# Kernel optimization log

Measured on AMD Instinct MI355X. Metric: run time of the kernel, lower is better.

## Reference

```python
import jax, jax.numpy as jnp
import numpy as np

NUM_USERS, NUM_ITEMS, D = 100000, 200000, 128
B, LLEN, SLEN = 4096, 200, 50
NEG = -1e9


def setup_inputs() -> dict:
    key = jax.random.key(0)
    ks = jax.random.split(key, 10)
    w_range = float(np.sqrt(3.0 / D))
    return {
        "user_table": 0.01 * jax.random.normal(ks[0], (NUM_USERS, D), dtype=jnp.float32),
        "item_table": 0.01 * jax.random.normal(ks[1], (NUM_ITEMS, D), dtype=jnp.float32),
        "W1": jax.random.uniform(ks[2], (2 * D, 16), minval=-w_range, maxval=w_range, dtype=jnp.float32),
        "b1": jnp.zeros((16,), dtype=jnp.float32),
        "W2": jax.random.uniform(ks[3], (16, 1), minval=-w_range, maxval=w_range, dtype=jnp.float32),
        "b2": jnp.zeros((1,), dtype=jnp.float32),
        "user_inputs": jax.random.randint(ks[4], (B,), 0, NUM_USERS, dtype=jnp.int64) if jax.config.jax_enable_x64 else jax.random.randint(ks[4], (B,), 0, NUM_USERS, dtype=jnp.int32),
        "L_inputs": jax.random.randint(ks[5], (B, LLEN), 0, NUM_ITEMS, dtype=jnp.int32),
        "S_inputs": jax.random.randint(ks[6], (B, SLEN), 0, NUM_ITEMS, dtype=jnp.int32),
        "item_inputs": jax.random.randint(ks[7], (B,), 0, NUM_ITEMS, dtype=jnp.int32),
    }


def reference(user_table, item_table, W1, b1, W2, b2,
              user_inputs, L_inputs, S_inputs, item_inputs):
    def att_logits(x):  # x: [..., 2D] -> [...]
        h = jax.nn.relu(x @ W1 + b1)
        return (h @ W2 + b2)[..., 0]

    def masked_softmax(logits, mask):  # softmax over last axis restricted to mask
        logits = jnp.where(mask, logits, NEG)
        return jax.nn.softmax(logits, axis=-1)

    u_emb = user_table[user_inputs]                      # [B, D]

    # ---- long-term attention over L history ----
    L_mask = L_inputs >= 0                               # [B, L]
    L_idx = jnp.where(L_mask, L_inputs, 0)
    L_emb = item_table[L_idx]                            # [B, L, D]
    uL = jnp.concatenate([jnp.broadcast_to(u_emb[:, None, :], L_emb.shape), L_emb], axis=-1)  # [B, L, 2D]
    w1 = masked_softmax(att_logits(uL), L_mask)          # [B, L]
    u_long = jnp.einsum('bl,bld->bd', w1, L_emb)         # [B, D]

    # ---- short-term attention over [u_long] + S (L assumed nonempty) ----
    S_mask = S_inputs >= 0                               # [B, S]
    S_idx = jnp.where(S_mask, S_inputs, 0)
    S_emb = item_table[S_idx]                            # [B, S, D]
    seq = jnp.concatenate([u_long[:, None, :], S_emb], axis=1)   # [B, 1+S, D]
    seq_mask = jnp.concatenate([jnp.ones((seq.shape[0], 1), dtype=bool), S_mask], axis=1)
    uSeq = jnp.concatenate([jnp.broadcast_to(u_emb[:, None, :], seq.shape), seq], axis=-1)  # [B, 1+S, 2D]
    w2 = masked_softmax(att_logits(uSeq), seq_mask)      # [B, 1+S]
    user_hybrid = jnp.einsum('bs,bsd->bd', w2, seq)      # [B, D]

    # ---- score: bmm([B,1,D], [B,D,1]) -> [B,1,1] ----
    item_emb = item_table[item_inputs]                   # [B, D]
    score = jnp.sum(user_hybrid * item_emb, axis=-1)[:, None, None]
    return score
```

## Files before the change

kernel.cpp:

```cpp
#include <hip/hip_runtime.h>
#include <math.h>

#define D 128
#define LLEN 200
#define SLEN 50
#define CH 64
#define ESTR 132
#define NEG (-1e9f)

__device__ __forceinline__ float wave_red_sum(float v) {
#pragma unroll
  for (int m = 32; m >= 1; m >>= 1) v += __shfl_xor(v, m, 64);
  return v;
}
__device__ __forceinline__ float block_sum(float v, float* red) {
  v = wave_red_sum(v);
  if ((threadIdx.x & 63) == 0) red[threadIdx.x >> 6] = v;
  __syncthreads();
  v = red[0] + red[1] + red[2] + red[3];
  __syncthreads();
  return v;
}

#define GATHER_L(dst, IT, BASE)                          \
  do {                                                   \
    int s_ = tid + (IT);                                 \
    int gid_ = rows1[(BASE) + (s_ >> 5)];                \
    if (gid_ < 0) gid_ = 0;                              \
    dst = it4[(size_t)gid_ * 32 + (s_ & 31)];            \
  } while (0)

#define GATHER_S(dst, IT)                                \
  do {                                                   \
    int s_ = tid + (IT);                                 \
    int gid_ = rowsS[s_ >> 5];                           \
    if (gid_ < 0) gid_ = 0;                              \
    dst = it4[(size_t)gid_ * 32 + (s_ & 31)];            \
  } while (0)

#define STORE_L(src, IT)                                                    \
  do {                                                                      \
    int s_ = tid + (IT);                                                    \
    reinterpret_cast<float4*>(&ebuf[(s_ >> 5) * ESTR])[s_ & 31] = src;      \
  } while (0)

#define STORE_S(src, IT)                                                    \
  do {                                                                      \
    int s_ = tid + (IT);                                                    \
    reinterpret_cast<float4*>(&ebuf[((s_ >> 5) + 1) * ESTR])[s_ & 31] = src; \
  } while (0)

#define MATVEC_PHASE(CNT)                                                   \
  if (lane < (CNT)) {                                                       \
    float a0 = 0.f, a1 = 0.f, a2 = 0.f, a3 = 0.f;                           \
    const float4* er4 = reinterpret_cast<const float4*>(&ebuf[lane * ESTR]);\
    const float* wc = &W1[(size_t)D * 16 + 4 * w];                          \
    _Pragma("unroll 8")                                                     \
    for (int k = 0; k < 32; ++k) {                                          \
      float4 e = er4[k];                                                    \
      const float* wr = wc + k * 64;            \
      a0 = fmaf(e.x, wr[0],  a0); a1 = fmaf(e.x, wr[1],  a1);               \
      a2 = fmaf(e.x, wr[2],  a2); a3 = fmaf(e.x, wr[3],  a3);               \
      a0 = fmaf(e.y, wr[16], a0); a1 = fmaf(e.y, wr[17], a1);               \
      a2 = fmaf(e.y, wr[18], a2); a3 = fmaf(e.y, wr[19], a3);               \
      a0 = fmaf(e.z, wr[32], a0); a1 = fmaf(e.z, wr[33], a1);               \
      a2 = fmaf(e.z, wr[34], a2); a3 = fmaf(e.z, wr[35], a3);               \
      a0 = fmaf(e.w, wr[48], a0); a1 = fmaf(e.w, wr[49], a1);               \
      a2 = fmaf(e.w, wr[50], a2); a3 = fmaf(e.w, wr[51], a3);               \
    }                                                                       \
    float hs = fmaxf(upart_sh[4 * w + 0] + a0, 0.f) * w2a;                  \
    hs = fmaf(fmaxf(upart_sh[4 * w + 1] + a1, 0.f), w2b, hs);               \
    hs = fmaf(fmaxf(upart_sh[4 * w + 2] + a2, 0.f), w2c, hs);               \
    hs = fmaf(fmaxf(upart_sh[4 * w + 3] + a3, 0.f), w2d, hs);               \
    hspart[w * 65 + lane] = hs;                                             \
  }

__global__ void __launch_bounds__(256, 4) din_kernel(
    const float* __restrict__ user_table, const float* __restrict__ item_table,
    const float* __restrict__ W1, const float* __restrict__ b1,
    const float* __restrict__ W2, const float* __restrict__ b2,
    const int* __restrict__ user_inputs, const int* __restrict__ L_inputs,
    const int* __restrict__ S_inputs, const int* __restrict__ item_inputs,
    float* __restrict__ out) {
  __shared__ float ebuf[CH * ESTR];
  __shared__ float hspart[4 * 65];
  __shared__ float w_sh[CH];
  __shared__ int rows1[LLEN];
  __shared__ int rowsS[SLEN];
  __shared__ float upart_sh[16];
  __shared__ float red_sh[4];

  const int b = blockIdx.x;
  const int tid = threadIdx.x;
  const int lane = tid & 63;
  const int w = __builtin_amdgcn_readfirstlane(tid >> 6);
  const int col4 = tid & 31;
  const int grp  = tid >> 5;
  const float4* it4 = reinterpret_cast<const float4*>(item_table);

  float* u_sh = &ebuf[0];
  float* part = &ebuf[128];
  if (tid < D) u_sh[tid] = user_table[(size_t)user_inputs[b] * D + tid];
  if (tid < LLEN) rows1[tid] = L_inputs[(size_t)b * LLEN + tid];
  if (tid < SLEN) rowsS[tid] = S_inputs[(size_t)b * SLEN + tid];
  __syncthreads();

  float4 p0, p1, p2, p3, p4, p5, p6, p7;
  GATHER_L(p0, 0,    0); GATHER_L(p1, 256,  0); GATHER_L(p2, 512,  0);
  GATHER_L(p3, 768,  0); GATHER_L(p4, 1024, 0); GATHER_L(p5, 1280, 0);
  GATHER_L(p6, 1536, 0); GATHER_L(p7, 1792, 0);

  {
    int j = tid & 15, g = tid >> 4;
    float p = 0.f;
#pragma unroll
    for (int t = 0; t < 8; ++t) {
      int d = g * 8 + t;
      p = fmaf(u_sh[d], W1[d * 16 + j], p);
    }
    part[tid] = p;
  }
  __syncthreads();
  if (tid < 16) {
    float s = b1[tid];
#pragma unroll
    for (int g = 0; g < 16; ++g) s += part[g * 16 + tid];
    upart_sh[tid] = s;
  }
  __syncthreads();

  const float b2v = b2[0];
  const float w2a = W2[4 * w + 0], w2b = W2[4 * w + 1];
  const float w2c = W2[4 * w + 2], w2d = W2[4 * w + 3];

  float pacc = 0.f;
  float4 uacc = make_float4(0.f, 0.f, 0.f, 0.f);

#pragma unroll
  for (int c = 0; c < 3; ++c) {
    const int base = c * CH;

    STORE_L(p0, 0);    STORE_L(p1, 256);  STORE_L(p2, 512);  STORE_L(p3, 768);
    STORE_L(p4, 1024); STORE_L(p5, 1280); STORE_L(p6, 1536); STORE_L(p7, 1792);
    __syncthreads();

    MATVEC_PHASE(64);
    __syncthreads();

    if (tid < 64) {
      float lg = hspart[tid] + hspart[65 + tid] + hspart[130 + tid] +
                 hspart[195 + tid] + b2v;
      float p = (rows1[base + tid] >= 0) ? expf(lg) : 0.f;
      w_sh[tid] = p;
      pacc += p;
    }
    __syncthreads();

    if (c < 2) {
      GATHER_L(p0, 0,    base + CH); GATHER_L(p1, 256,  base + CH);
      GATHER_L(p2, 512,  base + CH); GATHER_L(p3, 768,  base + CH);
      GATHER_L(p4, 1024, base + CH); GATHER_L(p5, 1280, base + CH);
      GATHER_L(p6, 1536, base + CH); GATHER_L(p7, 1792, base + CH);
    } else {
      GATHER_L(p0, 0, 192);
      GATHER_S(p1, 0);    GATHER_S(p2, 256);  GATHER_S(p3, 512);
      GATHER_S(p4, 768);  GATHER_S(p5, 1024); GATHER_S(p6, 1280);
      if (tid < 64) GATHER_S(p7, 1536);
    }

#pragma unroll
    for (int l8 = 0; l8 < 8; ++l8) {
      int l = grp + l8 * 8;
      float wl = w_sh[l];
      const float4 e = reinterpret_cast<const float4*>(&ebuf[l * ESTR])[col4];
      uacc.x = fmaf(wl, e.x, uacc.x);
      uacc.y = fmaf(wl, e.y, uacc.y);
      uacc.z = fmaf(wl, e.z, uacc.z);
      uacc.w = fmaf(wl, e.w, uacc.w);
    }
    __syncthreads();
  }

  STORE_L(p0, 0);
  __syncthreads();
  MATVEC_PHASE(8);
  __syncthreads();
  if (tid < 8) {
    float lg = hspart[tid] + hspart[65 + tid] + hspart[130 + tid] +
               hspart[195 + tid] + b2v;
    float p = (rows1[192 + tid] >= 0) ? expf(lg) : 0.f;
    w_sh[tid] = p;
    pacc += p;
  }
  __syncthreads();
  {
    float wl = w_sh[grp];
    const float4 e = reinterpret_cast<const float4*>(&ebuf[grp * ESTR])[col4];
    uacc.x = fmaf(wl, e.x, uacc.x);
    uacc.y = fmaf(wl, e.y, uacc.y);
    uacc.z = fmaf(wl, e.z, uacc.z);
    uacc.w = fmaf(wl, e.w, uacc.w);
  }

  const float invS1 = 1.f / block_sum(pacc, red_sh);
  float* scr = &ebuf[52 * ESTR];
  reinterpret_cast<float4*>(scr)[tid] = uacc;
  __syncthreads();
  if (tid < D) {
    float s = 0.f;
#pragma unroll
    for (int g = 0; g < 8; ++g) s += scr[g * 128 + tid];
    ebuf[tid] = s * invS1;
  }
  STORE_S(p1, 0);    STORE_S(p2, 256);  STORE_S(p3, 512);
  STORE_S(p4, 768);  STORE_S(p5, 1024); STORE_S(p6, 1280);
  if (tid < 64) STORE_S(p7, 1536);
  __syncthreads();

  const int n2 = 1 + SLEN;
  MATVEC_PHASE(n2);
  __syncthreads();

  float p2v = 0.f;
  if (tid < n2) {
    float lg = hspart[tid] + hspart[65 + tid] + hspart[130 + tid] +
               hspart[195 + tid] + b2v;
    bool valid = (tid == 0) || (rowsS[tid - 1] >= 0);
    p2v = valid ? expf(lg) : 0.f;
    w_sh[tid] = p2v;
  }
  const float invS2 = 1.f / block_sum(p2v, red_sh);

  float4 uacc2 = make_float4(0.f, 0.f, 0.f, 0.f);
  for (int l = grp; l < n2; l += 8) {
    float wl = w_sh[l];
    const float4 e = reinterpret_cast<const float4*>(&ebuf[l * ESTR])[col4];
    uacc2.x = fmaf(wl, e.x, uacc2.x);
    uacc2.y = fmaf(wl, e.y, uacc2.y);
    uacc2.z = fmaf(wl, e.z, uacc2.z);
    uacc2.w = fmaf(wl, e.w, uacc2.w);
  }
  reinterpret_cast<float4*>(scr)[tid] = uacc2;
  __syncthreads();

  float sv = 0.f;
  if (tid < D) {
    float s = 0.f;
#pragma unroll
    for (int g = 0; g < 8; ++g) s += scr[g * 128 + tid];
    float uh = s * invS2;
    sv = uh * item_table[(size_t)item_inputs[b] * D + tid];
  }
  float tot = block_sum(sv, red_sh);
  if (tid == 0) out[b] = tot;
}

extern "C" void kernel_launch(void* const* d_in, const int* in_sizes, int n_in,
                              void* d_out, int out_size, void* d_ws, size_t ws_size,
                              hipStream_t stream) {
  const float* user_table = (const float*)d_in[0];
  const float* item_table = (const float*)d_in[1];
  const float* W1 = (const float*)d_in[2];
  const float* b1 = (const float*)d_in[3];
  const float* W2 = (const float*)d_in[4];
  const float* b2 = (const float*)d_in[5];
  const int* user_inputs = (const int*)d_in[6];
  const int* L_inputs = (const int*)d_in[7];
  const int* S_inputs = (const int*)d_in[8];
  const int* item_inputs = (const int*)d_in[9];
  float* out = (float*)d_out;

  const int B = in_sizes[6];
  din_kernel<<<B, 256, 0, stream>>>(user_table, item_table, W1, b1, W2, b2,
                                    user_inputs, L_inputs, S_inputs, item_inputs,
                                    out);
}
```

Measured before the change: 269.5 us.

## Double-buffer gathers in registers and weight-sum from registers, raise occupancy

Splits the 200-row L history into chunks of 56 and double-buffers the gathered rows in two register sets (A/B). The next chunk's global loads are issued while the current chunk's matvec runs, and the weighted sum reads the embeddings straight from registers instead of re-reading shared memory. The launch-bounds occupancy target goes from 4 to 5, the item-embedding load is hoisted to kernel start, and the cross-group reduction now uses a shuffle before a smaller shared-memory pass. The cost is much higher register pressure (14 float4 buffers) alongside the higher occupancy target, which risks spills.

```diff
diff --git a/kernel.cpp b/kernel.cpp
--- a/kernel.cpp
+++ b/kernel.cpp
@@ -4,9 +4,8 @@
 #define D 128
 #define LLEN 200
 #define SLEN 50
-#define CH 64
+#define CH 56
 #define ESTR 132
-#define NEG (-1e9f)
 
 __device__ __forceinline__ float wave_red_sum(float v) {
 #pragma unroll
@@ -22,35 +21,43 @@
   return v;
 }
 
-#define GATHER_L(dst, IT, BASE)                          \
-  do {                                                   \
-    int s_ = tid + (IT);                                 \
-    int gid_ = rows1[(BASE) + (s_ >> 5)];                \
-    if (gid_ < 0) gid_ = 0;                              \
-    dst = it4[(size_t)gid_ * 32 + (s_ & 31)];            \
+#define GATHER_L(dst, IT, BASE)                        \
+  do {                                                 \
+    int s_ = tid + (IT);                               \
+    int gid_ = rows1[(BASE) + (s_ >> 5)];              \
+    if (gid_ < 0) gid_ = 0;                            \
+    dst = it4[(size_t)gid_ * 32 + (s_ & 31)];          \
   } while (0)
 
-#define GATHER_S(dst, IT)                                \
-  do {                                                   \
-    int s_ = tid + (IT);                                 \
-    int gid_ = rowsS[s_ >> 5];                           \
-    if (gid_ < 0) gid_ = 0;                              \
-    dst = it4[(size_t)gid_ * 32 + (s_ & 31)];            \
+#define GATHER_S(dst, IT)                              \
+  do {                                                 \
+    int s_ = tid + (IT);                               \
+    int gid_ = rowsS[s_ >> 5];                         \
+    if (gid_ < 0) gid_ = 0;                            \
+    dst = it4[(size_t)gid_ * 32 + (s_ & 31)];          \
   } while (0)
 
-#define STORE_L(src, IT)                                                    \
-  do {                                                                      \
-    int s_ = tid + (IT);                                                    \
-    reinterpret_cast<float4*>(&ebuf[(s_ >> 5) * ESTR])[s_ & 31] = src;      \
+#define STORE_L(src, IT)                                                     \
+  do {                                                                       \
+    int s_ = tid + (IT);                                                     \
+    reinterpret_cast<float4*>(&ebuf[(s_ >> 5) * ESTR])[s_ & 31] = src;       \
   } while (0)
 
-#define STORE_S(src, IT)                                                    \
-  do {                                                                      \
-    int s_ = tid + (IT);                                                    \
+#define STORE_S(src, IT)                                                     \
+  do {                                                                       \
+    int s_ = tid + (IT);                                                     \
     reinterpret_cast<float4*>(&ebuf[((s_ >> 5) + 1) * ESTR])[s_ & 31] = src; \
   } while (0)
 
-#define MATVEC_PHASE(CNT)                                                   \
+#define FMA4(WL, P, ACC)                \
+  do {                                  \
+    ACC.x = fmaf((WL), P.x, ACC.x);     \
+    ACC.y = fmaf((WL), P.y, ACC.y);     \
+    ACC.z = fmaf((WL), P.z, ACC.z);     \
+  } while (0);                          \
+  ACC.w = fmaf((WL), P.w, ACC.w)
+
+#define MATVEC_HS(CNT)                                                      \
   if (lane < (CNT)) {                                                       \
     float a0 = 0.f, a1 = 0.f, a2 = 0.f, a3 = 0.f;                           \
     const float4* er4 = reinterpret_cast<const float4*>(&ebuf[lane * ESTR]);\
@@ -75,7 +82,16 @@
     hspart[w * 65 + lane] = hs;                                             \
   }
 
-__global__ void __launch_bounds__(256, 4) din_kernel(
+#define FINALIZE_L(CNT, BASE)                                           \
+  if (tid < (CNT)) {                                                    \
+    float lg = hspart[tid] + hspart[65 + tid] + hspart[130 + tid] +     \
+               hspart[195 + tid] + b2v;                                 \
+    float p_ = (rows1[(BASE) + tid] >= 0) ? expf(lg) : 0.f;             \
+    w_sh[tid] = p_;                                                     \
+    pacc += p_;                                                         \
+  }
+
+__global__ void __launch_bounds__(256, 5) din_kernel(
     const float* __restrict__ user_table, const float* __restrict__ item_table,
     const float* __restrict__ W1, const float* __restrict__ b1,
     const float* __restrict__ W2, const float* __restrict__ b2,
@@ -95,20 +111,22 @@
   const int lane = tid & 63;
   const int w = __builtin_amdgcn_readfirstlane(tid >> 6);
   const int col4 = tid & 31;
-  const int grp  = tid >> 5;
+  const int grp = tid >> 5;
   const float4* it4 = reinterpret_cast<const float4*>(item_table);
 
   float* u_sh = &ebuf[0];
   float* part = &ebuf[128];
   if (tid < D) u_sh[tid] = user_table[(size_t)user_inputs[b] * D + tid];
+  const float item_f =
+      (tid < D) ? item_table[(size_t)item_inputs[b] * D + tid] : 0.f;
   if (tid < LLEN) rows1[tid] = L_inputs[(size_t)b * LLEN + tid];
   if (tid < SLEN) rowsS[tid] = S_inputs[(size_t)b * SLEN + tid];
   __syncthreads();
 
-  float4 p0, p1, p2, p3, p4, p5, p6, p7;
-  GATHER_L(p0, 0,    0); GATHER_L(p1, 256,  0); GATHER_L(p2, 512,  0);
-  GATHER_L(p3, 768,  0); GATHER_L(p4, 1024, 0); GATHER_L(p5, 1280, 0);
-  GATHER_L(p6, 1536, 0); GATHER_L(p7, 1792, 0);
+  float4 A0, A1, A2, A3, A4, A5, A6, B0, B1, B2, B3, B4, B5, B6;
+  GATHER_L(A0, 0, 0);    GATHER_L(A1, 256, 0);  GATHER_L(A2, 512, 0);
+  GATHER_L(A3, 768, 0);  GATHER_L(A4, 1024, 0); GATHER_L(A5, 1280, 0);
+  GATHER_L(A6, 1536, 0);
 
   {
     int j = tid & 15, g = tid >> 4;
@@ -135,121 +153,131 @@
 
   float pacc = 0.f;
   float4 uacc = make_float4(0.f, 0.f, 0.f, 0.f);
-
-#pragma unroll
-  for (int c = 0; c < 3; ++c) {
-    const int base = c * CH;
-
-    STORE_L(p0, 0);    STORE_L(p1, 256);  STORE_L(p2, 512);  STORE_L(p3, 768);
-    STORE_L(p4, 1024); STORE_L(p5, 1280); STORE_L(p6, 1536); STORE_L(p7, 1792);
-    __syncthreads();
-
-    MATVEC_PHASE(64);
-    __syncthreads();
-
-    if (tid < 64) {
-      float lg = hspart[tid] + hspart[65 + tid] + hspart[130 + tid] +
-                 hspart[195 + tid] + b2v;
-      float p = (rows1[base + tid] >= 0) ? expf(lg) : 0.f;
-      w_sh[tid] = p;
-      pacc += p;
-    }
-    __syncthreads();
-
-    if (c < 2) {
-      GATHER_L(p0, 0,    base + CH); GATHER_L(p1, 256,  base + CH);
-      GATHER_L(p2, 512,  base + CH); GATHER_L(p3, 768,  base + CH);
-      GATHER_L(p4, 1024, base + CH); GATHER_L(p5, 1280, base + CH);
-      GATHER_L(p6, 1536, base + CH); GATHER_L(p7, 1792, base + CH);
-    } else {
-      GATHER_L(p0, 0, 192);
-      GATHER_S(p1, 0);    GATHER_S(p2, 256);  GATHER_S(p3, 512);
-      GATHER_S(p4, 768);  GATHER_S(p5, 1024); GATHER_S(p6, 1280);
-      if (tid < 64) GATHER_S(p7, 1536);
-    }
-
-#pragma unroll
-    for (int l8 = 0; l8 < 8; ++l8) {
-      int l = grp + l8 * 8;
-      float wl = w_sh[l];
-      const float4 e = reinterpret_cast<const float4*>(&ebuf[l * ESTR])[col4];
-      uacc.x = fmaf(wl, e.x, uacc.x);
-      uacc.y = fmaf(wl, e.y, uacc.y);
-      uacc.z = fmaf(wl, e.z, uacc.z);
-      uacc.w = fmaf(wl, e.w, uacc.w);
-    }
-    __syncthreads();
-  }
-
-  STORE_L(p0, 0);
-  __syncthreads();
-  MATVEC_PHASE(8);
-  __syncthreads();
-  if (tid < 8) {
-    float lg = hspart[tid] + hspart[65 + tid] + hspart[130 + tid] +
-               hspart[195 + tid] + b2v;
-    float p = (rows1[192 + tid] >= 0) ? expf(lg) : 0.f;
-    w_sh[tid] = p;
-    pacc += p;
-  }
-  __syncthreads();
-  {
-    float wl = w_sh[grp];
-    const float4 e = reinterpret_cast<const float4*>(&ebuf[grp * ESTR])[col4];
-    uacc.x = fmaf(wl, e.x, uacc.x);
-    uacc.y = fmaf(wl, e.y, uacc.y);
-    uacc.z = fmaf(wl, e.z, uacc.z);
-    uacc.w = fmaf(wl, e.w, uacc.w);
-  }
+  float wl;
+
+  STORE_L(A0, 0);    STORE_L(A1, 256);  STORE_L(A2, 512);  STORE_L(A3, 768);
+  STORE_L(A4, 1024); STORE_L(A5, 1280); STORE_L(A6, 1536);
+  __syncthreads();
+  MATVEC_HS(56);
+  GATHER_L(B0, 0, 56);    GATHER_L(B1, 256, 56);  GATHER_L(B2, 512, 56);
+  GATHER_L(B3, 768, 56);  GATHER_L(B4, 1024, 56); GATHER_L(B5, 1280, 56);
+  GATHER_L(B6, 1536, 56);
+  __syncthreads();
+  FINALIZE_L(56, 0);
+  __syncthreads();
+  wl = w_sh[grp];      FMA4(wl, A0, uacc);
+  wl = w_sh[grp + 8];  FMA4(wl, A1, uacc);
+  wl = w_sh[grp + 16]; FMA4(wl, A2, uacc);
+  wl = w_sh[grp + 24]; FMA4(wl, A3, uacc);
+  wl = w_sh[grp + 32]; FMA4(wl, A4, uacc);
+  wl = w_sh[grp + 40]; FMA4(wl, A5, uacc);
+  wl = w_sh[grp + 48]; FMA4(wl, A6, uacc);
+
+  STORE_L(B0, 0);    STORE_L(B1, 256);  STORE_L(B2, 512);  STORE_L(B3, 768);
+  STORE_L(B4, 1024); STORE_L(B5, 1280); STORE_L(B6, 1536);
+  __syncthreads();
+  MATVEC_HS(56);
+  GATHER_L(A0, 0, 112);    GATHER_L(A1, 256, 112);  GATHER_L(A2, 512, 112);
+  GATHER_L(A3, 768, 112);  GATHER_L(A4, 1024, 112); GATHER_L(A5, 1280, 112);
+  GATHER_L(A6, 1536, 112);
+  __syncthreads();
+  FINALIZE_L(56, 56);
+  __syncthreads();
+  wl = w_sh[grp];      FMA4(wl, B0, uacc);
+  wl = w_sh[grp + 8];  FMA4(wl, B1, uacc);
+  wl = w_sh[grp + 16]; FMA4(wl, B2, uacc);
+  wl = w_sh[grp + 24]; FMA4(wl, B3, uacc);
+  wl = w_sh[grp + 32]; FMA4(wl, B4, uacc);
+  wl = w_sh[grp + 40]; FMA4(wl, B5, uacc);
+  wl = w_sh[grp + 48]; FMA4(wl, B6, uacc);
+
+  STORE_L(A0, 0);    STORE_L(A1, 256);  STORE_L(A2, 512);  STORE_L(A3, 768);
+  STORE_L(A4, 1024); STORE_L(A5, 1280); STORE_L(A6, 1536);
+  __syncthreads();
+  MATVEC_HS(56);
+  GATHER_L(B0, 0, 168); GATHER_L(B1, 256, 168);
+  GATHER_L(B2, 512, 168); GATHER_L(B3, 768, 168);
+  __syncthreads();
+  FINALIZE_L(56, 112);
+  __syncthreads();
+  wl = w_sh[grp];      FMA4(wl, A0, uacc);
+  wl = w_sh[grp + 8];  FMA4(wl, A1, uacc);
+  wl = w_sh[grp + 16]; FMA4(wl, A2, uacc);
+  wl = w_sh[grp + 24]; FMA4(wl, A3, uacc);
+  wl = w_sh[grp + 32]; FMA4(wl, A4, uacc);
+  wl = w_sh[grp + 40]; FMA4(wl, A5, uacc);
+  wl = w_sh[grp + 48]; FMA4(wl, A6, uacc);
+
+  STORE_L(B0, 0); STORE_L(B1, 256); STORE_L(B2, 512); STORE_L(B3, 768);
+  __syncthreads();
+  MATVEC_HS(32);
+  GATHER_S(A0, 0);    GATHER_S(A1, 256);  GATHER_S(A2, 512);
+  GATHER_S(A3, 768);  GATHER_S(A4, 1024); GATHER_S(A5, 1280);
+  if (tid < 64) GATHER_S(A6, 1536);
+  __syncthreads();
+  FINALIZE_L(32, 168);
+  __syncthreads();
+  wl = w_sh[grp];      FMA4(wl, B0, uacc);
+  wl = w_sh[grp + 8];  FMA4(wl, B1, uacc);
+  wl = w_sh[grp + 16]; FMA4(wl, B2, uacc);
+  wl = w_sh[grp + 24]; FMA4(wl, B3, uacc);
 
   const float invS1 = 1.f / block_sum(pacc, red_sh);
+  uacc.x += __shfl_xor(uacc.x, 32, 64);
+  uacc.y += __shfl_xor(uacc.y, 32, 64);
+  uacc.z += __shfl_xor(uacc.z, 32, 64);
+  uacc.w += __shfl_xor(uacc.w, 32, 64);
   float* scr = &ebuf[52 * ESTR];
-  reinterpret_cast<float4*>(scr)[tid] = uacc;
+  if (lane < 32) reinterpret_cast<float4*>(scr)[(w << 5) + lane] = uacc;
+  STORE_S(A0, 0);    STORE_S(A1, 256);  STORE_S(A2, 512);
+  STORE_S(A3, 768);  STORE_S(A4, 1024); STORE_S(A5, 1280);
+  if (tid < 64) STORE_S(A6, 1536);
   __syncthreads();
   if (tid < D) {
-    float s = 0.f;
-#pragma unroll
-    for (int g = 0; g < 8; ++g) s += scr[g * 128 + tid];
+    float s = scr[tid] + scr[128 + tid] + scr[256 + tid] + scr[384 + tid];
     ebuf[tid] = s * invS1;
   }
-  STORE_S(p1, 0);    STORE_S(p2, 256);  STORE_S(p3, 512);
-  STORE_S(p4, 768);  STORE_S(p5, 1024); STORE_S(p6, 1280);
-  if (tid < 64) STORE_S(p7, 1536);
-  __syncthreads();
-
-  const int n2 = 1 + SLEN;
-  MATVEC_PHASE(n2);
-  __syncthreads();
-
-  float p2v = 0.f;
-  if (tid < n2) {
+  __syncthreads();
+
+  MATVEC_HS(51);
+  __syncthreads();
+  float pacc2 = 0.f;
+  if (tid < 51) {
     float lg = hspart[tid] + hspart[65 + tid] + hspart[130 + tid] +
                hspart[195 + tid] + b2v;
     bool valid = (tid == 0) || (rowsS[tid - 1] >= 0);
-    p2v = valid ? expf(lg) : 0.f;
-    w_sh[tid] = p2v;
-  }
-  const float invS2 = 1.f / block_sum(p2v, red_sh);
+    float p_ = valid ? expf(lg) : 0.f;
+    w_sh[tid] = p_;
+    pacc2 = p_;
+  }
+  __syncthreads();
 
   float4 uacc2 = make_float4(0.f, 0.f, 0.f, 0.f);
-  for (int l = grp; l < n2; l += 8) {
-    float wl = w_sh[l];
-    const float4 e = reinterpret_cast<const float4*>(&ebuf[l * ESTR])[col4];
-    uacc2.x = fmaf(wl, e.x, uacc2.x);
-    uacc2.y = fmaf(wl, e.y, uacc2.y);
-    uacc2.z = fmaf(wl, e.z, uacc2.z);
-    uacc2.w = fmaf(wl, e.w, uacc2.w);
-  }
-  reinterpret_cast<float4*>(scr)[tid] = uacc2;
+  if (grp == 0) {
+    float wl0 = w_sh[0];
+    const float4 e = reinterpret_cast<const float4*>(&ebuf[0])[col4];
+    FMA4(wl0, e, uacc2);
+  }
+  wl = w_sh[1 + grp];      FMA4(wl, A0, uacc2);
+  wl = w_sh[1 + grp + 8];  FMA4(wl, A1, uacc2);
+  wl = w_sh[1 + grp + 16]; FMA4(wl, A2, uacc2);
+  wl = w_sh[1 + grp + 24]; FMA4(wl, A3, uacc2);
+  wl = w_sh[1 + grp + 32]; FMA4(wl, A4, uacc2);
+  wl = w_sh[1 + grp + 40]; FMA4(wl, A5, uacc2);
+  if (grp < 2) { wl = w_sh[1 + grp + 48]; FMA4(wl, A6, uacc2); }
+
+  const float invS2 = 1.f / block_sum(pacc2, red_sh);
+  uacc2.x += __shfl_xor(uacc2.x, 32, 64);
+  uacc2.y += __shfl_xor(uacc2.y, 32, 64);
+  uacc2.z += __shfl_xor(uacc2.z, 32, 64);
+  uacc2.w += __shfl_xor(uacc2.w, 32, 64);
+  if (lane < 32) reinterpret_cast<float4*>(scr)[(w << 5) + lane] = uacc2;
   __syncthreads();
 
   float sv = 0.f;
   if (tid < D) {
-    float s = 0.f;
-#pragma unroll
-    for (int g = 0; g < 8; ++g) s += scr[g * 128 + tid];
-    float uh = s * invS2;
-    sv = uh * item_table[(size_t)item_inputs[b] * D + tid];
+    float s = scr[tid] + scr[128 + tid] + scr[256 + tid] + scr[384 + tid];
+    sv = s * invS2 * item_f;
   }
   float tot = block_sum(sv, red_sh);
   if (tid == 0) out[b] = tot;
```

Result: faster. 256.5 us (-4.8%).
